# Optimization experiments

Hardware: AMD Instinct MI355X
Metric: run time of the kernel (lower is better)

Reference implementation:

```python
import jax, jax.numpy as jnp
import numpy as np

NUM_HEADS = 8


def setup_inputs() -> dict:
    key = jax.random.key(0)
    ks = jax.random.split(key, 6)
    B, C, H, W = 64, 512, 16, 16
    x = jax.random.normal(ks[0], (B, C, H, W), dtype=jnp.float32)
    qkv_w = jax.random.normal(ks[1], (3 * C, C), dtype=jnp.float32) * (C ** -0.5)
    qkv_b = jax.random.normal(ks[2], (3 * C,), dtype=jnp.float32) * 0.02
    out_w = jax.random.normal(ks[3], (C, C), dtype=jnp.float32) * (C ** -0.5)
    out_b = jax.random.normal(ks[4], (C,), dtype=jnp.float32) * 0.02
    rel_pos_enc = jax.random.normal(ks[5], (NUM_HEADS, 2 * 16 - 1, 2 * 16 - 1), dtype=jnp.float32) * 0.02
    return {"x": x, "qkv_w": qkv_w, "qkv_b": qkv_b, "out_w": out_w,
            "out_b": out_b, "rel_pos_enc": rel_pos_enc}


def _attention(x, qkv_w, qkv_b, out_w, out_b, rel_pos_enc):
    B, C, H, W = x.shape
    heads = rel_pos_enc.shape[0]
    hd = C // heads
    N = H * W

    # 1x1 conv qkv projection == pointwise GEMM over channels
    qkv = jnp.einsum('bchw,oc->bohw', x, qkv_w) + qkv_b[None, :, None, None]
    q, k, v = jnp.split(qkv, 3, axis=1)  # each (B, C, H, W)
    q = q.reshape(B, heads, hd, N)
    k = k.reshape(B, heads, hd, N)
    v = v.reshape(B, heads, hd, N)

    attn = jnp.einsum('bhdn,bhdm->bhnm', q, k) * (hd ** -0.5)  # (B,h,N,N)

    # gathered 2D relative position bias: bias[head,(h1,w1),(h2,w2)] =
    #   rel_pos_enc[head, h1-h2+15, w1-w2+15]
    h_idx = (jnp.arange(H)[:, None] - jnp.arange(H)[None, :]) + 16 - 1  # (H,H)
    w_idx = (jnp.arange(W)[:, None] - jnp.arange(W)[None, :]) + 16 - 1  # (W,W)
    bias = rel_pos_enc[:, h_idx[:, None, :, None], w_idx[None, :, None, :]]  # (h,H,W,H,W)
    bias = bias.reshape(heads, N, N)

    attn = jax.nn.softmax(attn + bias[None], axis=-1)
    out = jnp.einsum('bhnm,bhdm->bhdn', attn, v).reshape(B, C, H, W)
    out = jnp.einsum('bchw,oc->bohw', out, out_w) + out_b[None, :, None, None]
    return out


def reference(x, qkv_w, qkv_b, out_w, out_b, rel_pos_enc):
    return _attention(x, qkv_w, qkv_b, out_w, out_b, rel_pos_enc)
```

## Files before the change

### kernel.cpp

```cpp
#include <hip/hip_runtime.h>

typedef __attribute__((ext_vector_type(8))) short short8;
typedef __attribute__((ext_vector_type(4))) float floatx4;

#define MFMA16(a,b,c) __builtin_amdgcn_mfma_f32_16x16x32_bf16((a),(b),(c),0,0,0)

static __device__ __forceinline__ unsigned short f2bf(float f){
    unsigned int u = __float_as_uint(f);
    u = (u + 0x7FFFu + ((u >> 16) & 1u)) >> 16;
    return (unsigned short)u;
}

static __device__ __forceinline__ void async16(const unsigned short* g, const unsigned short* l){
    __builtin_amdgcn_global_load_lds(
        (const __attribute__((address_space(1))) unsigned int*)g,
        (__attribute__((address_space(3))) unsigned int*)l, 16, 0, 0);
}

__global__ __launch_bounds__(256) void k_prep(const float* __restrict__ x,
                                              unsigned short* __restrict__ xT,
                                              const float* __restrict__ qkvw,
                                              unsigned short* __restrict__ wqkv,
                                              const float* __restrict__ outw,
                                              unsigned short* __restrict__ wout){
    __shared__ unsigned short tile[64][72];
    const int bid = blockIdx.x;
    const int tid = threadIdx.x;
    if (bid < 2048){
        const int c0 = (bid & 7) * 64;
        const int n0 = ((bid >> 3) & 3) * 64;
        const int b  = bid >> 5;
        const int chunk = tid & 7;
        const int r     = tid >> 3;
        const float*    src = x  + (size_t)b * 131072;
        unsigned short* dst = xT + (size_t)b * 131072;
#pragma unroll
        for (int it = 0; it < 2; ++it){
            int c = r + it * 32;
            const float* p = src + (size_t)(c0 + c) * 256 + n0 + chunk * 8;
            float4 f0 = *(const float4*)(p);
            float4 f1 = *(const float4*)(p + 4);
            short8 v;
            v[0]=(short)f2bf(f0.x); v[1]=(short)f2bf(f0.y); v[2]=(short)f2bf(f0.z); v[3]=(short)f2bf(f0.w);
            v[4]=(short)f2bf(f1.x); v[5]=(short)f2bf(f1.y); v[6]=(short)f2bf(f1.z); v[7]=(short)f2bf(f1.w);
            *(short8*)&tile[c][chunk * 8] = v;
        }
        __syncthreads();
#pragma unroll
        for (int it = 0; it < 2; ++it){
            int n = r + it * 32;
            short8 o;
#pragma unroll
            for (int e = 0; e < 8; ++e) o[e] = (short)tile[chunk * 8 + e][n];
            *(short8*)(dst + (size_t)(n0 + n) * 512 + c0 + chunk * 8) = o;
        }
    } else {
        int i = (bid - 2048) * 256 + tid;
        const float* s; unsigned short* d; int j;
        if (i < 196608){ s = qkvw; d = wqkv; j = i; }
        else { j = i - 196608; if (j >= 65536) return; s = outw; d = wout; }
        float4 f = *(const float4*)(s + (size_t)j * 4);
        uint2 v;
        v.x = (unsigned int)f2bf(f.x) | ((unsigned int)f2bf(f.y) << 16);
        v.y = (unsigned int)f2bf(f.z) | ((unsigned int)f2bf(f.w) << 16);
        *(uint2*)(d + (size_t)j * 4) = v;
    }
}

__global__ __launch_bounds__(512, 2) void k_fused(const unsigned short* __restrict__ xT,
                                                  const unsigned short* __restrict__ wbf,
                                                  const float* __restrict__ qkvb,
                                                  const float* __restrict__ rel,
                                                  unsigned short* __restrict__ ao){
    __shared__ unsigned short SH[79748];
    const int XS = 0;
    const int WS = 16384;
    const int QS = 28672;
    const int KS = 45056;
    const int VS = 61440;
    float* Relsh = (float*)&SH[77824];

    const int bid  = blockIdx.x;
    const int xcd  = bid & 7;
    const int slot = bid >> 3;
    const int b = xcd * 8 + (slot & 7);
    const int h = slot >> 3;
    const int tid  = threadIdx.x;
    const int wave = tid >> 6;
    const int lane = tid & 63;
    const int lrow = lane & 15;
    const int lgrp = lane >> 4;
    const int mq = wave >> 1;
    const int nh = wave & 1;

    for (int i = tid; i < 961; i += 512) Relsh[i] = rel[h * 961 + i];

    floatx4 acc[4][6];
#pragma unroll
    for (int i = 0; i < 4; ++i)
#pragma unroll
        for (int j = 0; j < 6; ++j){ floatx4 z = {0.f,0.f,0.f,0.f}; acc[i][j] = z; }

    const unsigned short* xb = xT + (size_t)(b * 256) * 512;
    const unsigned short* xsrc[4]; int xdo[4];
#pragma unroll
    for (int c = 0; c < 4; ++c){
        int s   = (c * 8 + wave) * 64 + lane;
        int row = s >> 3, pch = s & 7;
        int sch = pch ^ (row & 7);
        xsrc[c] = xb + (size_t)row * 512 + sch * 8;
        xdo[c]  = (c * 8 + wave) * 512;
    }
    const unsigned short* wsrc[3]; int wdo[3];
#pragma unroll
    for (int c = 0; c < 3; ++c){
        int s   = (c * 8 + wave) * 64 + lane;
        int row = s >> 3, pch = s & 7;
        int sch = pch ^ (row & 7);
        int grow = (row >> 6) * 512 + h * 64 + (row & 63);
        wsrc[c] = wbf + (size_t)grow * 512 + sch * 8;
        wdo[c]  = (c * 8 + wave) * 512;
    }

    auto stageA = [&](int XBs, int WBs, int kk){
#pragma unroll
        for (int c = 0; c < 4; ++c) async16(xsrc[c] + kk, &SH[XBs + xdo[c]]);
#pragma unroll
        for (int c = 0; c < 3; ++c) async16(wsrc[c] + kk, &SH[WBs + wdo[c]]);
    };
    auto compA = [&](int XBs, int WBs){
#pragma unroll
        for (int ks = 0; ks < 2; ++ks){
            short8 af[4], bq[6];
#pragma unroll
            for (int mt = 0; mt < 4; ++mt){
                int row = mq * 64 + mt * 16 + lrow;
                int pch = (ks * 4 + lgrp) ^ (row & 7);
                af[mt] = *(const short8*)&SH[XBs + row * 64 + pch * 8];
            }
#pragma unroll
            for (int nt = 0; nt < 6; ++nt){
                int row = nh * 96 + nt * 16 + lrow;
                int pch = (ks * 4 + lgrp) ^ (row & 7);
                bq[nt] = *(const short8*)&SH[WBs + row * 64 + pch * 8];
            }
#pragma unroll
            for (int mt = 0; mt < 4; ++mt)
#pragma unroll
                for (int nt = 0; nt < 6; ++nt)
                    acc[mt][nt] = MFMA16(af[mt], bq[nt], acc[mt][nt]);
        }
    };

    stageA(XS, WS, 0);
    __syncthreads();
#pragma unroll
    for (int t2 = 0; t2 < 4; ++t2){
        stageA(QS, KS, t2 * 128 + 64);
        compA(XS, WS);
        __syncthreads();
        if (t2 < 3) stageA(XS, WS, t2 * 128 + 128);
        compA(QS, KS);
        __syncthreads();
    }

#pragma unroll
    for (int mt = 0; mt < 4; ++mt){
#pragma unroll
        for (int nt = 0; nt < 6; ++nt){
            int col = nh * 96 + nt * 16 + lrow;
            int seg = col >> 6, off = col & 63;
            float bv = qkvb[seg * 512 + h * 64 + off];
#pragma unroll
            for (int r = 0; r < 4; ++r){
                int token = mq * 64 + mt * 16 + lgrp * 4 + r;
                unsigned short v = f2bf(acc[mt][nt][r] + bv);
                if (seg == 2){
                    int lch = token >> 3;
                    int pch = (lch & 24) | ((lch & 7) ^ (off & 7));
                    SH[VS + off * 256 + pch * 8 + (token & 7)] = v;
                } else {
                    int base = seg ? KS : QS;
                    int pch  = (off >> 3) ^ (token & 7);
                    SH[base + token * 64 + pch * 8 + (off & 7)] = v;
                }
            }
        }
    }
    __syncthreads();

    short8 aq[2][2];
#pragma unroll
    for (int pp = 0; pp < 2; ++pp)
#pragma unroll
        for (int kc = 0; kc < 2; ++kc){
            int row = wave * 32 + pp * 16 + lrow;
            int pch = (kc * 4 + lgrp) ^ (row & 7);
            aq[pp][kc] = *(const short8*)&SH[QS + row * 64 + pch * 8];
        }

    floatx4 s2[2][16];
#pragma unroll
    for (int pp = 0; pp < 2; ++pp)
#pragma unroll
        for (int ct = 0; ct < 16; ++ct){
            int row = ct * 16 + lrow;
            int pch0 = lgrp ^ (row & 7);
            short8 b0 = *(const short8*)&SH[KS + row * 64 + pch0 * 8];
            short8 b1 = *(const short8*)&SH[KS + row * 64 + (pch0 ^ 4) * 8];
            floatx4 z = {0.f,0.f,0.f,0.f};
            z = MFMA16(aq[pp][0], b0, z);
            z = MFMA16(aq[pp][1], b1, z);
            s2[pp][ct] = z;
        }

    float inv[2][4];
#pragma unroll
    for (int pp = 0; pp < 2; ++pp)
#pragma unroll
        for (int r = 0; r < 4; ++r){
            int n   = wave * 32 + pp * 16 + lgrp * 4 + r;
            int nh_ = n >> 4, nw = n & 15;
            float sum = 0.f;
#pragma unroll
            for (int ct = 0; ct < 16; ++ct){
                float e = __expf(s2[pp][ct][r] * 0.125f +
                                 Relsh[(nh_ - ct + 15) * 31 + (nw - lrow + 15)]);
                s2[pp][ct][r] = e;
                sum += e;
            }
#pragma unroll
            for (int off = 1; off < 16; off <<= 1)
                sum += __shfl_xor(sum, off, 64);
            inv[pp][r] = 1.f / sum;
        }

    __syncthreads();

    const int PB = QS + wave * 4096;
    unsigned short* aob = ao + (size_t)(b * 256) * 512 + h * 64;
#pragma unroll
    for (int pp = 0; pp < 2; ++pp){
#pragma unroll
        for (int ct = 0; ct < 16; ++ct)
#pragma unroll
            for (int r = 0; r < 4; ++r){
                int row = lgrp * 4 + r;
                int lch = ct * 2 + (lrow >> 3);
                int pch = (lch & 24) | ((lch & 7) ^ (row & 7));
                SH[PB + row * 256 + pch * 8 + (lrow & 7)] = f2bf(s2[pp][ct][r]);
            }
        short8 pa[8];
#pragma unroll
        for (int ms = 0; ms < 8; ++ms){
            int lch = ms * 4 + lgrp;
            int pch = (lch & 24) | ((lch & 7) ^ (lrow & 7));
            pa[ms] = *(const short8*)&SH[PB + lrow * 256 + pch * 8];
        }
#pragma unroll
        for (int dt = 0; dt < 4; ++dt){
            floatx4 accO = {0.f,0.f,0.f,0.f};
#pragma unroll
            for (int ms = 0; ms < 8; ++ms){
                int row = dt * 16 + lrow;
                int lch = ms * 4 + lgrp;
                int pch = (lch & 24) | ((lch & 7) ^ (row & 7));
                short8 vb = *(const short8*)&SH[VS + row * 256 + pch * 8];
                accO = MFMA16(pa[ms], vb, accO);
            }
#pragma unroll
            for (int r = 0; r < 4; ++r){
                int n = wave * 32 + pp * 16 + lgrp * 4 + r;
                aob[(size_t)n * 512 + dt * 16 + lrow] = f2bf(accO[r] * inv[pp][r]);
            }
        }
    }
}

__global__ __launch_bounds__(256, 2) void k_out(const unsigned short* __restrict__ ao,
                                                const unsigned short* __restrict__ wbf,
                                                const float* __restrict__ bias,
                                                float* __restrict__ out){
    __shared__ unsigned short Ash[2][2][128][32];
    __shared__ unsigned short Bsh[2][2][128][32];
    const int bid  = blockIdx.x;
    const int xcd  = bid & 7;
    const int slot = bid >> 3;
    const int t0 = (xcd * 16 + (slot & 15)) * 128;
    const int o0 = (slot >> 4) * 128;
    const int tid  = threadIdx.x;
    const int wave = tid >> 6;
    const int lane = tid & 63;
    const int lrow = lane & 15;
    const int lk8  = (lane >> 4) * 8;
    const int wm   = (wave >> 1) * 64;
    const int wn   = (wave & 1) * 64;
    const int ld_row = wave * 32 + (lane >> 2);
    const int ld_col = (lane & 3) * 8;

    floatx4 acc[4][4];
#pragma unroll
    for (int i = 0; i < 4; ++i)
#pragma unroll
        for (int j = 0; j < 4; ++j){ floatx4 z = {0.f,0.f,0.f,0.f}; acc[i][j] = z; }

    const unsigned short* gA = wbf + (size_t)(o0 + ld_row) * 512 + ld_col;
    const unsigned short* gB = ao  + (size_t)(t0 + ld_row) * 512 + ld_col;

    auto stage = [&](int d, int kk){
        async16(gA + kk,                 &Ash[d][0][wave * 32][0]);
        async16(gA + kk + 16 * 512,      &Ash[d][0][wave * 32 + 16][0]);
        async16(gA + kk + 32,            &Ash[d][1][wave * 32][0]);
        async16(gA + kk + 32 + 16 * 512, &Ash[d][1][wave * 32 + 16][0]);
        async16(gB + kk,                 &Bsh[d][0][wave * 32][0]);
        async16(gB + kk + 16 * 512,      &Bsh[d][0][wave * 32 + 16][0]);
        async16(gB + kk + 32,            &Bsh[d][1][wave * 32][0]);
        async16(gB + kk + 32 + 16 * 512, &Bsh[d][1][wave * 32 + 16][0]);
    };
    auto comp = [&](int d){
#pragma unroll
        for (int s = 0; s < 2; ++s){
            short8 af[4], bq[4];
#pragma unroll
            for (int mt = 0; mt < 4; ++mt) af[mt] = *(const short8*)&Ash[d][s][wm + mt*16 + lrow][lk8];
#pragma unroll
            for (int nt = 0; nt < 4; ++nt) bq[nt] = *(const short8*)&Bsh[d][s][wn + nt*16 + lrow][lk8];
#pragma unroll
            for (int mt = 0; mt < 4; ++mt)
#pragma unroll
                for (int nt = 0; nt < 4; ++nt)
                    acc[mt][nt] = MFMA16(af[mt], bq[nt], acc[mt][nt]);
        }
    };

    stage(0, 0);
    __syncthreads();
#pragma unroll
    for (int t2 = 0; t2 < 4; ++t2){
        stage(1, t2 * 128 + 64);
        comp(0);
        __syncthreads();
        if (t2 < 3) stage(0, t2 * 128 + 128);
        comp(1);
        __syncthreads();
    }
#pragma unroll
    for (int mt = 0; mt < 4; ++mt){
        int orow0 = o0 + wm + mt*16 + (lane >> 4) * 4;
#pragma unroll
        for (int nt = 0; nt < 4; ++nt){
            int tcol = t0 + wn + nt*16 + lrow;
            int bb = tcol >> 8, nn = tcol & 255;
#pragma unroll
            for (int r = 0; r < 4; ++r){
                float bv = bias[orow0 + r];
                out[(size_t)(bb * 512 + orow0 + r) * 256 + nn] = acc[mt][nt][r] + bv;
            }
        }
    }
}

extern "C" void kernel_launch(void* const* d_in, const int* in_sizes, int n_in,
                              void* d_out, int out_size, void* d_ws, size_t ws_size,
                              hipStream_t stream){
    const float* x    = (const float*)d_in[0];
    const float* qkvw = (const float*)d_in[1];
    const float* qkvb = (const float*)d_in[2];
    const float* outw = (const float*)d_in[3];
    const float* outb = (const float*)d_in[4];
    const float* rel  = (const float*)d_in[5];
    float* out = (float*)d_out;

    const size_t XT_OFF = 0;
    const size_t AO_OFF = 16777216;
    const size_t W_OFF  = 33554432;
    const size_t NEED   = W_OFF + 4194304;
    if (ws_size < NEED) return;

    char* ws = (char*)d_ws;
    unsigned short* xT = (unsigned short*)(ws + XT_OFF);
    unsigned short* ao = (unsigned short*)(ws + AO_OFF);
    unsigned short* wqkv_bf = (unsigned short*)(ws + W_OFF);
    unsigned short* wout_bf = (unsigned short*)(ws + W_OFF + 2097152);

    hipLaunchKernelGGL(k_prep,  dim3(3072), dim3(256), 0, stream,
                       x, xT, qkvw, wqkv_bf, outw, wout_bf);
    hipLaunchKernelGGL(k_fused, dim3(512),  dim3(512), 0, stream,
                       xT, wqkv_bf, qkvb, rel, ao);
    hipLaunchKernelGGL(k_out,   dim3(512),  dim3(256), 0, stream,
                       ao, wout_bf, outb, out);
}
```

Baseline: 156.6 us.

## Keep softmax probabilities in registers, fold scales into exp2, swizzle LDS in out-proj

```diff
diff --git a/kernel.cpp b/kernel.cpp
--- a/kernel.cpp
+++ b/kernel.cpp
@@ -2,6 +2,7 @@
 
 typedef __attribute__((ext_vector_type(8))) short short8;
 typedef __attribute__((ext_vector_type(4))) float floatx4;
+typedef __attribute__((ext_vector_type(4))) int   intx4;
 
 #define MFMA16(a,b,c) __builtin_amdgcn_mfma_f32_16x16x32_bf16((a),(b),(c),0,0,0)
 
@@ -9,6 +10,12 @@
     unsigned int u = __float_as_uint(f);
     u = (u + 0x7FFFu + ((u >> 16) & 1u)) >> 16;
     return (unsigned short)u;
+}
+
+static __device__ __forceinline__ unsigned int pkbf(float lo, float hi){
+    unsigned int r;
+    asm("v_cvt_pk_bf16_f32 %0, %1, %2" : "=v"(r) : "v"(lo), "v"(hi));
+    return r;
 }
 
 static __device__ __forceinline__ void async16(const unsigned short* g, const unsigned short* l){
@@ -23,7 +30,7 @@
                                               unsigned short* __restrict__ wqkv,
                                               const float* __restrict__ outw,
                                               unsigned short* __restrict__ wout){
-    __shared__ unsigned short tile[64][72];
+    __shared__ unsigned short tile[64][78];
     const int bid = blockIdx.x;
     const int tid = threadIdx.x;
     if (bid < 2048){
@@ -93,7 +100,7 @@
     const int mq = wave >> 1;
     const int nh = wave & 1;
 
-    for (int i = tid; i < 961; i += 512) Relsh[i] = rel[h * 961 + i];
+    for (int i = tid; i < 961; i += 512) Relsh[i] = rel[h * 961 + i] * 1.44269504f;
 
     floatx4 acc[4][6];
 #pragma unroll
@@ -171,18 +178,29 @@
             int col = nh * 96 + nt * 16 + lrow;
             int seg = col >> 6, off = col & 63;
             float bv = qkvb[seg * 512 + h * 64 + off];
-#pragma unroll
-            for (int r = 0; r < 4; ++r){
-                int token = mq * 64 + mt * 16 + lgrp * 4 + r;
-                unsigned short v = f2bf(acc[mt][nt][r] + bv);
-                if (seg == 2){
-                    int lch = token >> 3;
-                    int pch = (lch & 24) | ((lch & 7) ^ (off & 7));
-                    SH[VS + off * 256 + pch * 8 + (token & 7)] = v;
-                } else {
-                    int base = seg ? KS : QS;
-                    int pch  = (off >> 3) ^ (token & 7);
-                    SH[base + token * 64 + pch * 8 + (off & 7)] = v;
+            int token0 = mq * 64 + mt * 16 + lgrp * 4;
+            if (seg == 2){
+                int lch = token0 >> 3;
+                int pch = (lch & 24) | ((lch & 7) ^ (off & 7));
+                uint2 vv;
+                vv.x = pkbf(acc[mt][nt][0] + bv, acc[mt][nt][1] + bv);
+                vv.y = pkbf(acc[mt][nt][2] + bv, acc[mt][nt][3] + bv);
+                *(uint2*)&SH[VS + off * 256 + pch * 8 + (lgrp & 1) * 4] = vv;
+            } else if (seg == 1){
+#pragma unroll
+                for (int r = 0; r < 4; ++r){
+                    int token = token0 + r;
+                    int kslot = (token & ~0x1C) | ((token & 4) << 2) | ((token & 0x18) >> 1);
+                    int pch   = (off >> 3) ^ (kslot & 7);
+                    SH[KS + kslot * 64 + pch * 8 + (off & 7)] = f2bf(acc[mt][nt][r] + bv);
+                }
+            } else {
+#pragma unroll
+                for (int r = 0; r < 4; ++r){
+                    int token = token0 + r;
+                    int pch   = (off >> 3) ^ (token & 7);
+                    SH[QS + token * 64 + pch * 8 + (off & 7)] =
+                        f2bf((acc[mt][nt][r] + bv) * 0.18033688f);
                 }
             }
         }
@@ -199,64 +217,56 @@
             aq[pp][kc] = *(const short8*)&SH[QS + row * 64 + pch * 8];
         }
 
-    floatx4 s2[2][16];
-#pragma unroll
-    for (int pp = 0; pp < 2; ++pp)
+    unsigned short* aob = ao + (size_t)(b * 256) * 512 + h * 64;
+    const int khB = lgrp >> 1;
+    const int kwB = (lgrp & 1) * 8;
+
+#pragma unroll
+    for (int pp = 0; pp < 2; ++pp){
+        floatx4 st[16];
+        __builtin_amdgcn_s_setprio(1);
 #pragma unroll
         for (int ct = 0; ct < 16; ++ct){
-            int row = ct * 16 + lrow;
+            int row  = ct * 16 + lrow;
             int pch0 = lgrp ^ (row & 7);
-            short8 b0 = *(const short8*)&SH[KS + row * 64 + pch0 * 8];
-            short8 b1 = *(const short8*)&SH[KS + row * 64 + (pch0 ^ 4) * 8];
+            short8 k0 = *(const short8*)&SH[KS + row * 64 + pch0 * 8];
+            short8 k1 = *(const short8*)&SH[KS + row * 64 + (pch0 ^ 4) * 8];
             floatx4 z = {0.f,0.f,0.f,0.f};
-            z = MFMA16(aq[pp][0], b0, z);
-            z = MFMA16(aq[pp][1], b1, z);
-            s2[pp][ct] = z;
-        }
-
-    float inv[2][4];
-#pragma unroll
-    for (int pp = 0; pp < 2; ++pp)
-#pragma unroll
-        for (int r = 0; r < 4; ++r){
-            int n   = wave * 32 + pp * 16 + lgrp * 4 + r;
-            int nh_ = n >> 4, nw = n & 15;
-            float sum = 0.f;
-#pragma unroll
-            for (int ct = 0; ct < 16; ++ct){
-                float e = __expf(s2[pp][ct][r] * 0.125f +
-                                 Relsh[(nh_ - ct + 15) * 31 + (nw - lrow + 15)]);
-                s2[pp][ct][r] = e;
+            z = MFMA16(k0, aq[pp][0], z);
+            z = MFMA16(k1, aq[pp][1], z);
+            st[ct] = z;
+        }
+        __builtin_amdgcn_s_setprio(0);
+
+        float sum = 0.f;
+        const int rbase = (wave * 2 + pp + 15) * 31 + lrow + 15 - kwB;
+#pragma unroll
+        for (int ct = 0; ct < 16; ++ct){
+            int rb = rbase - (2 * (ct >> 1) + khB) * 31 - 4 * (ct & 1);
+#pragma unroll
+            for (int r = 0; r < 4; ++r){
+                float e = __builtin_amdgcn_exp2f(st[ct][r] + Relsh[rb - r]);
+                st[ct][r] = e;
                 sum += e;
             }
-#pragma unroll
-            for (int off = 1; off < 16; off <<= 1)
-                sum += __shfl_xor(sum, off, 64);
-            inv[pp][r] = 1.f / sum;
-        }
-
-    __syncthreads();
-
-    const int PB = QS + wave * 4096;
-    unsigned short* aob = ao + (size_t)(b * 256) * 512 + h * 64;
-#pragma unroll
-    for (int pp = 0; pp < 2; ++pp){
-#pragma unroll
-        for (int ct = 0; ct < 16; ++ct)
-#pragma unroll
-            for (int r = 0; r < 4; ++r){
-                int row = lgrp * 4 + r;
-                int lch = ct * 2 + (lrow >> 3);
-                int pch = (lch & 24) | ((lch & 7) ^ (row & 7));
-                SH[PB + row * 256 + pch * 8 + (lrow & 7)] = f2bf(s2[pp][ct][r]);
-            }
-        short8 pa[8];
+        }
+        sum += __shfl_xor(sum, 16, 64);
+        sum += __shfl_xor(sum, 32, 64);
+        float inv = 1.f / sum;
+
+        intx4 pf[8];
 #pragma unroll
         for (int ms = 0; ms < 8; ++ms){
-            int lch = ms * 4 + lgrp;
-            int pch = (lch & 24) | ((lch & 7) ^ (lrow & 7));
-            pa[ms] = *(const short8*)&SH[PB + lrow * 256 + pch * 8];
-        }
+            intx4 t;
+            t.x = (int)pkbf(st[2*ms  ][0], st[2*ms  ][1]);
+            t.y = (int)pkbf(st[2*ms  ][2], st[2*ms  ][3]);
+            t.z = (int)pkbf(st[2*ms+1][0], st[2*ms+1][1]);
+            t.w = (int)pkbf(st[2*ms+1][2], st[2*ms+1][3]);
+            pf[ms] = t;
+        }
+
+        const int n = wave * 32 + pp * 16 + lrow;
+        __builtin_amdgcn_s_setprio(1);
 #pragma unroll
         for (int dt = 0; dt < 4; ++dt){
             floatx4 accO = {0.f,0.f,0.f,0.f};
@@ -266,14 +276,14 @@
                 int lch = ms * 4 + lgrp;
                 int pch = (lch & 24) | ((lch & 7) ^ (row & 7));
                 short8 vb = *(const short8*)&SH[VS + row * 256 + pch * 8];
-                accO = MFMA16(pa[ms], vb, accO);
-            }
-#pragma unroll
-            for (int r = 0; r < 4; ++r){
-                int n = wave * 32 + pp * 16 + lgrp * 4 + r;
-                aob[(size_t)n * 512 + dt * 16 + lrow] = f2bf(accO[r] * inv[pp][r]);
-            }
-        }
+                accO = MFMA16(vb, __builtin_bit_cast(short8, pf[ms]), accO);
+            }
+            uint2 ov;
+            ov.x = pkbf(accO[0] * inv, accO[1] * inv);
+            ov.y = pkbf(accO[2] * inv, accO[3] * inv);
+            *(uint2*)(aob + (size_t)n * 512 + dt * 16 + lgrp * 4) = ov;
+        }
+        __builtin_amdgcn_s_setprio(0);
     }
 }
 
@@ -292,11 +302,11 @@
     const int wave = tid >> 6;
     const int lane = tid & 63;
     const int lrow = lane & 15;
-    const int lk8  = (lane >> 4) * 8;
     const int wm   = (wave >> 1) * 64;
     const int wn   = (wave & 1) * 64;
     const int ld_row = wave * 32 + (lane >> 2);
-    const int ld_col = (lane & 3) * 8;
+    const int ld_col = (((lane & 3) ^ ((lane >> 3) & 3))) * 8;
+    const int pcho = (((lane >> 4) ^ ((lrow >> 1) & 3))) * 8;
 
     floatx4 acc[4][4];
 #pragma unroll
@@ -322,9 +332,9 @@
         for (int s = 0; s < 2; ++s){
             short8 af[4], bq[4];
 #pragma unroll
-            for (int mt = 0; mt < 4; ++mt) af[mt] = *(const short8*)&Ash[d][s][wm + mt*16 + lrow][lk8];
-#pragma unroll
-            for (int nt = 0; nt < 4; ++nt) bq[nt] = *(const short8*)&Bsh[d][s][wn + nt*16 + lrow][lk8];
+            for (int mt = 0; mt < 4; ++mt) af[mt] = *(const short8*)&Ash[d][s][wm + mt*16 + lrow][pcho];
+#pragma unroll
+            for (int nt = 0; nt < 4; ++nt) bq[nt] = *(const short8*)&Bsh[d][s][wn + nt*16 + lrow][pcho];
 #pragma unroll
             for (int mt = 0; mt < 4; ++mt)
 #pragma unroll
```

Result: faster. 151.2 us (-3.4%).
